# Kernel tuning notes

Hardware: AMD Instinct MI355X
Metric: run time of the kernel (lower is better)

Reference implementation:

```python
import jax, jax.numpy as jnp
import numpy as np

TAO = 3
M = 5
C_IN = 7
D_MODEL = 512
KERNELS = D_MODEL // C_IN          # 73
EXTRA = D_MODEL - C_IN * KERNELS   # 1


def _circular_conv1d(x_nct, w_oik, b_o):
    # Conv1d(kernel_size=3, padding=1, padding_mode='circular') == wrap-pad by 1 then VALID conv.
    xp = jnp.pad(x_nct, ((0, 0), (0, 0), (1, 1)), mode='wrap')
    out = jax.lax.conv_general_dilated(
        xp, w_oik, window_strides=(1,), padding='VALID',
        dimension_numbers=('NCH', 'OIH', 'NCH'))
    return out + b_o[None, :, None]


def setup_inputs() -> dict:
    key = jax.random.key(0)
    k1, k2, k3 = jax.random.split(key, 3)
    B, S = 32, 4096
    x = jax.random.normal(k1, (B, S, C_IN), dtype=jnp.float32)
    # kaiming_normal fan_in for Conv1d(in=m+1, k=3): std = sqrt(2/(1+0.01**2)) / sqrt((M+1)*3)
    std = float(np.sqrt(2.0 / (1.0 + 0.01 ** 2)) / np.sqrt((M + 1) * 3))
    w_conv = jax.random.normal(k2, (KERNELS, M + 1, 3), dtype=jnp.float32) * std
    b_conv = jnp.zeros((KERNELS,), dtype=jnp.float32)
    w_left = jax.random.normal(k3, (EXTRA, M + 1, 3), dtype=jnp.float32) * std
    b_left = jnp.zeros((EXTRA,), dtype=jnp.float32)
    return {"x": x, "w_conv": w_conv, "b_conv": b_conv, "w_left": w_left, "b_left": b_left}


def reference(x, w_conv, b_conv, w_left, b_left):
    B, S, C = x.shape
    L = S - M * TAO
    # time-delay gather: faithful vectors [x[t], x[t-tao], ..., x[t-m*tao]] per channel
    valid_t = jnp.arange(M * TAO, S)
    offs = jnp.arange(M + 1) * TAO
    idx = valid_t[:, None] - offs[None, :]            # [L, m+1]
    ext = x[:, idx, :]                                # [B, L, m+1, C]
    ext = jnp.transpose(ext, (0, 1, 3, 2))            # [B, L, C, m+1] (channel-major)
    emb = ext.reshape(B, L, C * (M + 1))
    emb = jnp.pad(emb, ((0, 0), (M * TAO, 0), (0, 0)))  # pad=True: left-pad time with zeros -> [B,S,C*(m+1)]
    # split into c_in chunks of (m+1) and run the SAME conv on each -> batch over (B*C)
    chunks = emb.reshape(B, S, C, M + 1).transpose(0, 2, 3, 1)  # [B, C, m+1, S]
    merged = chunks.reshape(B * C, M + 1, S)
    out = _circular_conv1d(merged, w_conv, b_conv)              # [B*C, K, S]
    out = out.reshape(B, C * KERNELS, S)                        # concat of per-chunk outputs
    # leftout conv on the LAST chunk only
    last = chunks[:, -1]                                        # [B, m+1, S]
    out_left = _circular_conv1d(last, w_left, b_left)           # [B, extra, S]
    out_full = jnp.concatenate([out, out_left], axis=1)         # [B, d_model, S]
    return jnp.transpose(out_full, (0, 2, 1))                   # [B, S, d_model]
```

## Files before the change

kernel.cpp:

```cpp
#include <hip/hip_runtime.h>

#define S     4096
#define CIN   7
#define DM    512
#define KERN  73
#define TT    256
#define TILES (S / TT)
#define TROW  276
#define CHUNK 8

__global__ __launch_bounds__(512, 4)
void tokemb_kernel(const float* __restrict__ x,
                   const float* __restrict__ w_conv,
                   const float* __restrict__ b_conv,
                   const float* __restrict__ w_left,
                   const float* __restrict__ b_left,
                   float* __restrict__ out)
{
    __shared__ float xs[CIN * TROW];

    const int blk  = blockIdx.x;
    const int b    = blk / TILES;
    const int tile = blk - b * TILES;
    const int t0   = tile * TT;
    const int d    = threadIdx.x;

    const int NE = CIN * (TT + 17);
    const float* xb = x + (long long)b * S * CIN;
    for (int e = d; e < NE; e += 512) {
        int j = e / CIN;
        int c = e - j * CIN;
        int tm = t0 - 16 + j;
        if (tm < 0) tm += S;
        else if (tm >= S) tm -= S;
        xs[c * TROW + j] = xb[tm * CIN + c];
    }

    const int cc = (d < DM - 1) ? (d / KERN) : (CIN - 1);
    const int oo = d % KERN;
    const float* wrow = (d < DM - 1) ? (w_conv + oo * 18) : w_left;
    const float bias  = (d < DM - 1) ? b_conv[oo] : b_left[0];
    float wt[18];
    #pragma unroll
    for (int q = 0; q < 18; ++q) wt[q] = wrow[q];

    __syncthreads();

    const float* xrow = xs + cc * TROW;
    float* op = out + ((long long)b * S + t0) * DM + d;

    for (int tt0 = 0; tt0 < TT; tt0 += CHUNK) {
        float win[28];
        #pragma unroll
        for (int q = 0; q < 7; ++q) {
            float4 v = *reinterpret_cast<const float4*>(xrow + tt0 + 4 * q);
            win[4*q+0] = v.x; win[4*q+1] = v.y;
            win[4*q+2] = v.z; win[4*q+3] = v.w;
        }

        float acc[CHUNK];
        const int tc = t0 + tt0;
        const bool edge = (tc < 16) || (tc + CHUNK >= S);
        if (!edge) {
            #pragma unroll
            for (int i = 0; i < CHUNK; ++i) {
                float a = bias;
                #pragma unroll
                for (int m = 0; m < 6; ++m) {
                    #pragma unroll
                    for (int k = 0; k < 3; ++k) {
                        a = fmaf(wt[m*3+k], win[i + k + 15 - 3*m], a);
                    }
                }
                acc[i] = a;
            }
        } else {
            #pragma unroll
            for (int i = 0; i < CHUNK; ++i) {
                float p0 = 0.f, p1 = 0.f, p2 = 0.f;
                #pragma unroll
                for (int m = 0; m < 6; ++m) {
                    p0 = fmaf(wt[m*3+0], win[i + 15 - 3*m], p0);
                    p1 = fmaf(wt[m*3+1], win[i + 16 - 3*m], p1);
                    p2 = fmaf(wt[m*3+2], win[i + 17 - 3*m], p2);
                }
                const int t = tc + i;
                const float f0 = (t == 0 || t >= 16)      ? 1.f : 0.f;
                const float f1 = (t >= 15)                ? 1.f : 0.f;
                const float f2 = (t >= 14 && t != S - 1)  ? 1.f : 0.f;
                acc[i] = bias + f0 * p0 + f1 * p1 + f2 * p2;
            }
        }

        #pragma unroll
        for (int i = 0; i < CHUNK; ++i) {
            __builtin_nontemporal_store(acc[i], op + (tt0 + i) * DM);
        }
    }
}

extern "C" void kernel_launch(void* const* d_in, const int* in_sizes, int n_in,
                              void* d_out, int out_size, void* d_ws, size_t ws_size,
                              hipStream_t stream) {
    const float* x      = (const float*)d_in[0];
    const float* w_conv = (const float*)d_in[1];
    const float* b_conv = (const float*)d_in[2];
    const float* w_left = (const float*)d_in[3];
    const float* b_left = (const float*)d_in[4];
    float* out = (float*)d_out;

    const int B = in_sizes[0] / (S * CIN);
    dim3 grid(B * TILES);
    tokemb_kernel<<<grid, 512, 0, stream>>>(x, w_conv, b_conv, w_left, b_left, out);
}
```

Measured before the change: 59.41 us.

## Give each thread four output channels and write results as float4 stores

Each thread now computes four adjacent output channels over a 32-step time slice instead of one channel over the whole tile. This allows 128-bit vectorized output stores in place of scalar nontemporal stores. The time tile is halved to 128, which doubles the grid, and the occupancy hint is lowered to fit the larger register footprint. The weights are pre-reordered into offset order to simplify the inner FMA loop, and edge handling is restricted to the blocks that need it. The cost is more registers per thread, plus the loss of the nontemporal hint and a larger relative halo-load overhead per tile.

```diff
diff --git a/kernel.cpp b/kernel.cpp
--- a/kernel.cpp
+++ b/kernel.cpp
@@ -1,15 +1,16 @@
 #include <hip/hip_runtime.h>
 
-#define S     4096
-#define CIN   7
-#define DM    512
-#define KERN  73
-#define TT    256
-#define TILES (S / TT)
-#define TROW  276
-#define CHUNK 8
+#define S      4096
+#define CIN    7
+#define DM     512
+#define KERN   73
+#define TT     128
+#define TILES  (S / TT)
+#define NSTAGE (TT + 17)
+#define TROW   148
+#define CHUNK  8
 
-__global__ __launch_bounds__(512, 4)
+__global__ __launch_bounds__(512, 2)
 void tokemb_kernel(const float* __restrict__ x,
                    const float* __restrict__ w_conv,
                    const float* __restrict__ b_conv,
@@ -20,81 +21,95 @@
     __shared__ float xs[CIN * TROW];
 
     const int blk  = blockIdx.x;
-    const int b    = blk / TILES;
-    const int tile = blk - b * TILES;
+    const int b    = blk >> 5;
+    const int tile = blk & (TILES - 1);
     const int t0   = tile * TT;
-    const int d    = threadIdx.x;
+    const int tid  = threadIdx.x;
 
-    const int NE = CIN * (TT + 17);
     const float* xb = x + (long long)b * S * CIN;
-    for (int e = d; e < NE; e += 512) {
-        int j = e / CIN;
-        int c = e - j * CIN;
+    for (int e = tid; e < CIN * NSTAGE; e += 512) {
+        int j = e / CIN, c = e - j * CIN;
         int tm = t0 - 16 + j;
-        if (tm < 0) tm += S;
-        else if (tm >= S) tm -= S;
+        if (tm < 0) tm += S; else if (tm >= S) tm -= S;
         xs[c * TROW + j] = xb[tm * CIN + c];
     }
 
-    const int cc = (d < DM - 1) ? (d / KERN) : (CIN - 1);
-    const int oo = d % KERN;
-    const float* wrow = (d < DM - 1) ? (w_conv + oo * 18) : w_left;
-    const float bias  = (d < DM - 1) ? b_conv[oo] : b_left[0];
-    float wt[18];
+    const int dq = tid & 127, d0 = 4 * dq;
+    const int tg = tid >> 7;
+
+    float g[4][18], bias[4];
+    int   row[4];
     #pragma unroll
-    for (int q = 0; q < 18; ++q) wt[q] = wrow[q];
+    for (int dd = 0; dd < 4; ++dd) {
+        const int d  = d0 + dd;
+        const int oo = d % KERN;
+        const float* wrow = (d < DM - 1) ? (w_conv + oo * 18) : w_left;
+        bias[dd] = (d < DM - 1) ? b_conv[oo] : b_left[0];
+        row[dd]  = (d < DM - 1) ? (d / KERN) : (CIN - 1);
+        #pragma unroll
+        for (int off = 0; off < 18; ++off)
+            g[dd][off] = wrow[(5 - off / 3) * 3 + (off % 3)];
+    }
 
     __syncthreads();
 
-    const float* xrow = xs + cc * TROW;
-    float* op = out + ((long long)b * S + t0) * DM + d;
+    const int tstart = t0 + tg * 32;
+    const int jbase  = tg * 32;
+    float* op = out + ((long long)b * S + tstart) * DM + d0;
 
-    for (int tt0 = 0; tt0 < TT; tt0 += CHUNK) {
-        float win[28];
-        #pragma unroll
-        for (int q = 0; q < 7; ++q) {
-            float4 v = *reinterpret_cast<const float4*>(xrow + tt0 + 4 * q);
-            win[4*q+0] = v.x; win[4*q+1] = v.y;
-            win[4*q+2] = v.z; win[4*q+3] = v.w;
-        }
+    const bool edgeblk = (tile == 0 && tg == 0) || (tile == TILES - 1 && tg == 3);
 
-        float acc[CHUNK];
-        const int tc = t0 + tt0;
-        const bool edge = (tc < 16) || (tc + CHUNK >= S);
+    for (int ch = 0; ch < 32; ch += CHUNK) {
+        float acc[4][CHUNK];
+        const int tc = tstart + ch;
+        const bool edge = edgeblk && ((tc < 16) || (tc + CHUNK >= S));
+
         if (!edge) {
             #pragma unroll
-            for (int i = 0; i < CHUNK; ++i) {
-                float a = bias;
+            for (int dd = 0; dd < 4; ++dd) {
+                const float* xw = xs + row[dd] * TROW + jbase + ch;
+                float w4[28];
                 #pragma unroll
-                for (int m = 0; m < 6; ++m) {
+                for (int q = 0; q < 7; ++q) {
+                    float4 v = *reinterpret_cast<const float4*>(xw + 4 * q);
+                    w4[4*q+0] = v.x; w4[4*q+1] = v.y;
+                    w4[4*q+2] = v.z; w4[4*q+3] = v.w;
+                }
+                #pragma unroll
+                for (int i = 0; i < CHUNK; ++i) {
+                    float a = bias[dd];
                     #pragma unroll
-                    for (int k = 0; k < 3; ++k) {
-                        a = fmaf(wt[m*3+k], win[i + k + 15 - 3*m], a);
-                    }
+                    for (int off = 0; off < 18; ++off)
+                        a = fmaf(g[dd][off], w4[i + off], a);
+                    acc[dd][i] = a;
                 }
-                acc[i] = a;
             }
         } else {
             #pragma unroll
-            for (int i = 0; i < CHUNK; ++i) {
-                float p0 = 0.f, p1 = 0.f, p2 = 0.f;
+            for (int dd = 0; dd < 4; ++dd) {
+                const float* xw = xs + row[dd] * TROW + jbase + ch;
                 #pragma unroll
-                for (int m = 0; m < 6; ++m) {
-                    p0 = fmaf(wt[m*3+0], win[i + 15 - 3*m], p0);
-                    p1 = fmaf(wt[m*3+1], win[i + 16 - 3*m], p1);
-                    p2 = fmaf(wt[m*3+2], win[i + 17 - 3*m], p2);
+                for (int i = 0; i < CHUNK; ++i) {
+                    float p0 = 0.f, p1 = 0.f, p2 = 0.f;
+                    #pragma unroll
+                    for (int o = 0; o < 18; o += 3) {
+                        p0 = fmaf(g[dd][o],     xw[i + o],     p0);
+                        p1 = fmaf(g[dd][o + 1], xw[i + o + 1], p1);
+                        p2 = fmaf(g[dd][o + 2], xw[i + o + 2], p2);
+                    }
+                    const int t = tc + i;
+                    const float f0 = (t == 0 || t >= 16)     ? 1.f : 0.f;
+                    const float f1 = (t >= 15)               ? 1.f : 0.f;
+                    const float f2 = (t >= 14 && t != S - 1) ? 1.f : 0.f;
+                    acc[dd][i] = bias[dd] + f0 * p0 + f1 * p1 + f2 * p2;
                 }
-                const int t = tc + i;
-                const float f0 = (t == 0 || t >= 16)      ? 1.f : 0.f;
-                const float f1 = (t >= 15)                ? 1.f : 0.f;
-                const float f2 = (t >= 14 && t != S - 1)  ? 1.f : 0.f;
-                acc[i] = bias + f0 * p0 + f1 * p1 + f2 * p2;
             }
         }
 
         #pragma unroll
         for (int i = 0; i < CHUNK; ++i) {
-            __builtin_nontemporal_store(acc[i], op + (tt0 + i) * DM);
+            float4 v = make_float4(acc[0][i], acc[1][i], acc[2][i], acc[3][i]);
+            *reinterpret_cast<float4*>(op + (ch + i) * DM) = v;
         }
     }
 }
```

Measured after the change: 62.69 us. 1.06x slower.
